# Kernel optimization log

Hardware: AMD Instinct MI355X
Metric: run time of the kernel (lower is better)

The kernel has to match this reference:

```python
import jax, jax.numpy as jnp
import numpy as np

T, B, IN, H, L = 128, 512, 512, 512, 2


def setup_inputs() -> dict:
    key = jax.random.key(0)
    ks = jax.random.split(key, 8)
    inp = {
        "latent": jax.random.normal(ks[0], (T, B, IN), jnp.float32),
        "h0": jax.random.normal(ks[1], (L, B, H), jnp.float32),
        "c0": jax.random.normal(ks[2], (L, B, H), jnp.float32),
        "reset_mask": jax.random.randint(ks[3], (T, B), 0, 2, jnp.int32),
    }
    # LSTM params, torch layout: W_ih (4H, in), W_hh (4H, H), biases (4H,) init to 1
    for l in range(L):
        in_l = IN if l == 0 else H
        k1, k2 = jax.random.split(jax.random.fold_in(key, 100 + l))
        inp[f"W_ih{l}"] = jax.random.normal(k1, (4 * H, in_l), jnp.float32) / np.float32(np.sqrt(in_l))
        inp[f"W_hh{l}"] = jax.random.normal(k2, (4 * H, H), jnp.float32) / np.float32(np.sqrt(H))
        inp[f"b_ih{l}"] = jnp.ones((4 * H,), jnp.float32)
        inp[f"b_hh{l}"] = jnp.ones((4 * H,), jnp.float32)
    return inp


def _cell(x, h, c, W_ih, W_hh, b_ih, b_hh):
    # torch gate order: input, forget, cell(g), output
    gates = x @ W_ih.T + b_ih + h @ W_hh.T + b_hh  # (B, 4H)
    i, f, g, o = jnp.split(gates, 4, axis=-1)
    i = jax.nn.sigmoid(i)
    f = jax.nn.sigmoid(f)
    g = jnp.tanh(g)
    o = jax.nn.sigmoid(o)
    c_new = f * c + i * g
    h_new = o * jnp.tanh(c_new)
    return h_new, c_new


def reference(latent, h0, c0, reset_mask,
              W_ih0, W_hh0, b_ih0, b_hh0,
              W_ih1, W_hh1, b_ih1, b_hh1):
    def step(carry, xs):
        h, c = carry  # (L, B, H) each
        x_t, m_t = xs
        m = (m_t != 0)[None, :, None]  # (1, B, 1), broadcast over layers and H
        h = jnp.where(m, 0.0, h)
        c = jnp.where(m, 0.0, c)
        h0n, c0n = _cell(x_t, h[0], c[0], W_ih0, W_hh0, b_ih0, b_hh0)
        h1n, c1n = _cell(h0n, h[1], c[1], W_ih1, W_hh1, b_ih1, b_hh1)
        return (jnp.stack([h0n, h1n]), jnp.stack([c0n, c1n])), h1n

    (h_n, c_n), hidden = jax.lax.scan(step, (h0, c0), (latent, reset_mask))
    return hidden, h_n, c_n  # hidden: (T, B, H)
```

## Files before the change

kernel.cpp:

```cpp
#include <hip/hip_runtime.h>
#include <hip/hip_bf16.h>

typedef __hip_bfloat16 bf16;
typedef unsigned short u16;
typedef unsigned long long u64;
using frag  = __attribute__((ext_vector_type(8))) short;
using f32x4 = __attribute__((ext_vector_type(4))) float;

static constexpr int T_  = 128;
static constexpr int B_  = 512;
static constexpr int H_  = 512;
static constexpr int K_  = 512;
static constexpr int G4_ = 2048;
static constexpr int NWG = 256;

static constexpr size_t W_BYTES = 131072;
static constexpr size_t SMEM_BYTES = W_BYTES;


__global__ void k_f32_to_bf16_v4(const float4* __restrict__ src,
                                 ushort4* __restrict__ dst, int n4) {
  int i = blockIdx.x * blockDim.x + threadIdx.x;
  int stride = gridDim.x * blockDim.x;
  for (; i < n4; i += stride) {
    float4 v = src[i];
    ushort4 o;
    bf16 t0 = __float2bfloat16(v.x); o.x = *reinterpret_cast<u16*>(&t0);
    bf16 t1 = __float2bfloat16(v.y); o.y = *reinterpret_cast<u16*>(&t1);
    bf16 t2 = __float2bfloat16(v.z); o.z = *reinterpret_cast<u16*>(&t2);
    bf16 t3 = __float2bfloat16(v.w); o.w = *reinterpret_cast<u16*>(&t3);
    dst[i] = o;
  }
}

__global__ void k_bias(const float* __restrict__ bih0, const float* __restrict__ bhh0,
                       const float* __restrict__ bih1, const float* __restrict__ bhh1,
                       float* __restrict__ bsum0, float* __restrict__ bsum1) {
  int i = blockIdx.x * blockDim.x + threadIdx.x;
  if (i < G4_) {
    bsum0[i] = bih0[i] + bhh0[i];
    bsum1[i] = bih1[i] + bhh1[i];
  }
}

__global__ void k_init2(const float* __restrict__ h0,
                        u16* __restrict__ bufA0, u16* __restrict__ bufA1) {
  int i = blockIdx.x * blockDim.x + threadIdx.x;
  int n = B_ * H_;
  if (i < n) {
    bf16 a = __float2bfloat16(h0[i]);
    bf16 b = __float2bfloat16(h0[n + i]);
    bufA0[i] = *reinterpret_cast<u16*>(&a);
    bufA1[n + i] = *reinterpret_cast<u16*>(&b);
  }
}

__global__ void k_zero(int* p) {
  int i = blockIdx.x * blockDim.x + threadIdx.x;
  if (i < 256) p[i] = 0;
}

__global__ __launch_bounds__(512, 2)
void k_main(const u16* __restrict__ latb,
            const u16* __restrict__ W0i, const u16* __restrict__ W0h,
            const u16* __restrict__ W1i, const u16* __restrict__ W1h,
            const float* __restrict__ bs0, const float* __restrict__ bs1,
            const int* __restrict__ reset,
            const float* __restrict__ c0,
            u16* __restrict__ h0seq,
            u16* __restrict__ bufA0,
            u16* __restrict__ bufA1,
            float* __restrict__ hidden,
            float* __restrict__ hn,
            float* __restrict__ cn,
            int* __restrict__ arr) {
  extern __shared__ char smem_raw[];
  u16* wlds = (u16*)smem_raw;
  __shared__ float hstage[8][16][20];

  const int tid   = threadIdx.x;
  const int wg    = blockIdx.x;
  const int lb    = wg & 7;
  const int layer = lb >> 2;
  const int bg    = lb & 3;
  const int cg    = wg >> 3;
  const int hbase = cg * 16;
  const int rowbase = bg * 128;
  const int wave  = tid >> 6;
  const int lane  = tid & 63;
  const int r16   = lane & 15;
  const int kq    = lane >> 4;
  const int wrow_local = wave * 16;
  const int wrow0 = rowbase + wrow_local;

  const u16* Wih = layer ? W1i : W0i;
  const u16* Whh = layer ? W1h : W0h;
  const float* bs = layer ? bs1 : bs0;
  u16* bufA_self = layer ? bufA1 : bufA0;

  for (int it = 0; it < 16; ++it) {
    int c = it * 512 + tid;
    int fb = c >> 6, l = c & 63;
    int ni = fb >> 5, kslot = fb & 31;
    int col = hbase + (l & 15);
    int klocal = (kslot & 15) * 32 + (l >> 4) * 8;
    const u16* M = (kslot < 16) ? Wih : Whh;
    const u16* src = M + (size_t)(ni * H_ + col) * K_ + klocal;
    *(float4*)(wlds + ((size_t)c) * 8) = *(const float4*)src;
  }

  float bias[4];
  #pragma unroll
  for (int g = 0; g < 4; ++g) bias[g] = bs[g * H_ + hbase + r16];

  float creg[4];
  #pragma unroll
  for (int j = 0; j < 4; ++j)
    creg[j] = c0[((size_t)layer * B_ + (wrow0 + kq * 4 + j)) * H_ + hbase + r16];

  __syncthreads();

  for (int p = 0; p <= T_; ++p) {
    if (p) { asm volatile("buffer_inv sc0" ::: "memory"); }

    const int t = layer ? (p - 1) : p;
    const bool active = (t >= 0 && t < T_);
    float hnew_r[4], cnew_r[4];

    if (active) {
      const u16* X  = layer ? (h0seq + (size_t)t * B_ * H_)
                            : (latb + (size_t)t * B_ * K_);
      const u16* Hp = bufA_self + (size_t)(p & 1) * B_ * H_;
      u16* HnA      = bufA_self + (size_t)((p + 1) & 1) * B_ * H_;

      const int* rst_t = reset + (size_t)t * B_;
      const int ra0 = rst_t[wrow0 + r16];
      const u16* x0  = X  + (size_t)(wrow0 + r16) * K_ + kq * 8;
      const u16* hp0 = Hp + (size_t)(wrow0 + r16) * H_ + kq * 8;

      f32x4 acc[4] = {};
      const frag zf = {};

      #pragma unroll
      for (int s = 0; s < 16; ++s) {
        frag a  = *reinterpret_cast<const frag*>(x0 + s * 32);
        frag ah = ra0 ? zf : *reinterpret_cast<const frag*>(hp0 + s * 32);
        #pragma unroll
        for (int ni = 0; ni < 4; ++ni) {
          frag bx = *reinterpret_cast<const frag*>(
              wlds + ((size_t)((ni * 32 + s) * 64 + lane)) * 8);
          frag bh = *reinterpret_cast<const frag*>(
              wlds + ((size_t)((ni * 32 + 16 + s) * 64 + lane)) * 8);
          acc[ni] = __builtin_amdgcn_mfma_f32_16x16x32_bf16(a,  bx, acc[ni], 0, 0, 0);
          acc[ni] = __builtin_amdgcn_mfma_f32_16x16x32_bf16(ah, bh, acc[ni], 0, 0, 0);
        }
      }

      #pragma unroll
      for (int j = 0; j < 4; ++j) {
        const int rstj = rst_t[wrow0 + kq * 4 + j];
        float gi = acc[0][j] + bias[0];
        float gf = acc[1][j] + bias[1];
        float gg = acc[2][j] + bias[2];
        float go = acc[3][j] + bias[3];
        float iv = 1.f / (1.f + __expf(-gi));
        float fv = 1.f / (1.f + __expf(-gf));
        float gv = 1.f - 2.f / (__expf(2.f * gg) + 1.f);
        float ov = 1.f / (1.f + __expf(-go));
        float ce = rstj ? 0.f : creg[j];
        float cnew = fv * ce + iv * gv;
        float hnew = ov * (1.f - 2.f / (__expf(2.f * cnew) + 1.f));
        creg[j] = cnew;
        cnew_r[j] = cnew;
        hnew_r[j] = hnew;
        hstage[wave][kq * 4 + j][r16] = hnew;
      }

      {
        const int prow = lane >> 2;
        const int pc4  = lane & 3;
        float4 v = *reinterpret_cast<const float4*>(&hstage[wave][prow][pc4 * 4]);
        bf16 b0 = __float2bfloat16(v.x), b1 = __float2bfloat16(v.y);
        bf16 b2 = __float2bfloat16(v.z), b3 = __float2bfloat16(v.w);
        u64 pk = (u64)*reinterpret_cast<u16*>(&b0)
               | ((u64)*reinterpret_cast<u16*>(&b1) << 16)
               | ((u64)*reinterpret_cast<u16*>(&b2) << 32)
               | ((u64)*reinterpret_cast<u16*>(&b3) << 48);
        const size_t hoff = (size_t)(wrow0 + prow) * H_ + hbase + pc4 * 4;
        *(u64*)(HnA + hoff) = pk;
        if (layer == 0) {
          __hip_atomic_store((u64*)(h0seq + (size_t)t * B_ * H_ + hoff), pk,
                             __ATOMIC_RELAXED, __HIP_MEMORY_SCOPE_AGENT);
        }
      }
    }

    if (p < T_) {
      asm volatile("s_waitcnt vmcnt(0)" ::: "memory");
      __syncthreads();
      if (tid == 0)
        __hip_atomic_store(arr + wg, p + 1, __ATOMIC_RELAXED, __HIP_MEMORY_SCOPE_AGENT);
    }

    if (active) {
      float* hidden_t = hidden + (size_t)t * B_ * H_;
      #pragma unroll
      for (int j = 0; j < 4; ++j) {
        const size_t off = (size_t)(wrow0 + kq * 4 + j) * H_ + hbase + r16;
        if (layer) hidden_t[off] = hnew_r[j];
        if (t == T_ - 1) {
          hn[(size_t)layer * B_ * H_ + off] = hnew_r[j];
          cn[(size_t)layer * B_ * H_ + off] = cnew_r[j];
        }
      }
    }

    if (p < T_) {
      if (wave == 0) {
        const int slot = (lane >> 1) * 8 + (lane & 1) * 4 + bg;
        while (__hip_atomic_load(arr + slot, __ATOMIC_RELAXED,
                                 __HIP_MEMORY_SCOPE_AGENT) < p + 1)
          __builtin_amdgcn_s_sleep(2);
      }
      __syncthreads();
    }
  }
}


extern "C" void kernel_launch(void* const* d_in, const int* in_sizes, int n_in,
                              void* d_out, int out_size, void* d_ws, size_t ws_size,
                              hipStream_t stream) {
  (void)in_sizes; (void)n_in; (void)out_size; (void)ws_size;

  const float* latent = (const float*)d_in[0];
  const float* h0in   = (const float*)d_in[1];
  const float* c0in   = (const float*)d_in[2];
  const int*   reset  = (const int*)d_in[3];
  const float* W_ih0  = (const float*)d_in[4];
  const float* W_hh0  = (const float*)d_in[5];
  const float* b_ih0  = (const float*)d_in[6];
  const float* b_hh0  = (const float*)d_in[7];
  const float* W_ih1  = (const float*)d_in[8];
  const float* W_hh1  = (const float*)d_in[9];
  const float* b_ih1  = (const float*)d_in[10];
  const float* b_hh1  = (const float*)d_in[11];

  float* out    = (float*)d_out;
  float* hidden = out;
  float* hn     = out + (size_t)T_ * B_ * H_;
  float* cn     = hn + (size_t)2 * B_ * H_;

  char* ws = (char*)d_ws;
  u16* latb  = (u16*)ws;
  u16* wih0b = latb + (size_t)T_ * B_ * K_;
  u16* whh0b = wih0b + (size_t)G4_ * K_;
  u16* wih1b = whh0b + (size_t)G4_ * K_;
  u16* whh1b = wih1b + (size_t)G4_ * K_;
  float* bsum0 = (float*)(whh1b + (size_t)G4_ * K_);
  float* bsum1 = bsum0 + G4_;
  u16* h0seq = (u16*)(bsum1 + G4_);
  u16* bufA0 = h0seq + (size_t)T_ * B_ * H_;
  u16* bufA1 = bufA0 + (size_t)2 * B_ * H_;
  int* arr   = (int*)(bufA1 + (size_t)2 * B_ * H_);

  int n_lat4 = T_ * B_ * K_ / 4;
  k_f32_to_bf16_v4<<<2048, 256, 0, stream>>>((const float4*)latent, (ushort4*)latb, n_lat4);
  int n_w4 = G4_ * K_ / 4;
  k_f32_to_bf16_v4<<<256, 256, 0, stream>>>((const float4*)W_ih0, (ushort4*)wih0b, n_w4);
  k_f32_to_bf16_v4<<<256, 256, 0, stream>>>((const float4*)W_hh0, (ushort4*)whh0b, n_w4);
  k_f32_to_bf16_v4<<<256, 256, 0, stream>>>((const float4*)W_ih1, (ushort4*)wih1b, n_w4);
  k_f32_to_bf16_v4<<<256, 256, 0, stream>>>((const float4*)W_hh1, (ushort4*)whh1b, n_w4);
  k_bias<<<(G4_ + 255) / 256, 256, 0, stream>>>(b_ih0, b_hh0, b_ih1, b_hh1, bsum0, bsum1);
  k_init2<<<(B_ * H_ + 255) / 256, 256, 0, stream>>>(h0in, bufA0, bufA1);
  k_zero<<<1, 256, 0, stream>>>(arr);

  hipFuncSetAttribute((const void*)k_main, hipFuncAttributeMaxDynamicSharedMemorySize,
                      (int)SMEM_BYTES);
  void* args[] = { (void*)&latb, (void*)&wih0b, (void*)&whh0b, (void*)&wih1b, (void*)&whh1b,
                   (void*)&bsum0, (void*)&bsum1, (void*)&reset, (void*)&c0in,
                   (void*)&h0seq, (void*)&bufA0, (void*)&bufA1,
                   (void*)&hidden, (void*)&hn, (void*)&cn, (void*)&arr };
  hipLaunchCooperativeKernel((void*)k_main, dim3(NWG), dim3(512), args,
                             (unsigned int)SMEM_BYTES, stream);
}
```

Before: 1.385 ms.

## Prefetch next-step input fragments into registers and narrow inter-layer barrier waits

```diff
diff --git a/kernel.cpp b/kernel.cpp
--- a/kernel.cpp
+++ b/kernel.cpp
@@ -98,6 +98,9 @@
   const float* bs = layer ? bs1 : bs0;
   u16* bufA_self = layer ? bufA1 : bufA0;
 
+  const int slotL0own = (lane & 31) * 8 + bg;
+  const int slotL1own = (lane & 31) * 8 + 4 + bg;
+
   for (int it = 0; it < 16; ++it) {
     int c = it * 512 + tid;
     int fb = c >> 6, l = c & 63;
@@ -118,6 +121,14 @@
   for (int j = 0; j < 4; ++j)
     creg[j] = c0[((size_t)layer * B_ + (wrow0 + kq * 4 + j)) * H_ + hbase + r16];
 
+  frag xfr[16];
+  if (layer == 0) {
+    const u16* x0 = latb + (size_t)(wrow0 + r16) * K_ + kq * 8;
+    #pragma unroll
+    for (int s = 0; s < 16; ++s)
+      xfr[s] = *reinterpret_cast<const frag*>(x0 + s * 32);
+  }
+
   __syncthreads();
 
   for (int p = 0; p <= T_; ++p) {
@@ -128,14 +139,11 @@
     float hnew_r[4], cnew_r[4];
 
     if (active) {
-      const u16* X  = layer ? (h0seq + (size_t)t * B_ * H_)
-                            : (latb + (size_t)t * B_ * K_);
       const u16* Hp = bufA_self + (size_t)(p & 1) * B_ * H_;
       u16* HnA      = bufA_self + (size_t)((p + 1) & 1) * B_ * H_;
 
       const int* rst_t = reset + (size_t)t * B_;
       const int ra0 = rst_t[wrow0 + r16];
-      const u16* x0  = X  + (size_t)(wrow0 + r16) * K_ + kq * 8;
       const u16* hp0 = Hp + (size_t)(wrow0 + r16) * H_ + kq * 8;
 
       f32x4 acc[4] = {};
@@ -143,7 +151,6 @@
 
       #pragma unroll
       for (int s = 0; s < 16; ++s) {
-        frag a  = *reinterpret_cast<const frag*>(x0 + s * 32);
         frag ah = ra0 ? zf : *reinterpret_cast<const frag*>(hp0 + s * 32);
         #pragma unroll
         for (int ni = 0; ni < 4; ++ni) {
@@ -151,8 +158,8 @@
               wlds + ((size_t)((ni * 32 + s) * 64 + lane)) * 8);
           frag bh = *reinterpret_cast<const frag*>(
               wlds + ((size_t)((ni * 32 + 16 + s) * 64 + lane)) * 8);
-          acc[ni] = __builtin_amdgcn_mfma_f32_16x16x32_bf16(a,  bx, acc[ni], 0, 0, 0);
-          acc[ni] = __builtin_amdgcn_mfma_f32_16x16x32_bf16(ah, bh, acc[ni], 0, 0, 0);
+          acc[ni] = __builtin_amdgcn_mfma_f32_16x16x32_bf16(xfr[s], bx, acc[ni], 0, 0, 0);
+          acc[ni] = __builtin_amdgcn_mfma_f32_16x16x32_bf16(ah,     bh, acc[ni], 0, 0, 0);
         }
       }
 
@@ -216,8 +223,28 @@
     }
 
     if (p < T_) {
+      const int tn = layer ? p : (p + 1);
+      const bool nact = (tn < T_);
+
+      if (layer == 1 && nact) {
+        if (wave == 0) {
+          while (__hip_atomic_load(arr + slotL0own, __ATOMIC_RELAXED,
+                                   __HIP_MEMORY_SCOPE_AGENT) < p + 1)
+            __builtin_amdgcn_s_sleep(2);
+        }
+        __syncthreads();
+      }
+      if (nact) {
+        const u16* X = layer ? (h0seq + (size_t)tn * B_ * H_)
+                             : (latb + (size_t)tn * B_ * K_);
+        const u16* x0 = X + (size_t)(wrow0 + r16) * K_ + kq * 8;
+        #pragma unroll
+        for (int s = 0; s < 16; ++s)
+          xfr[s] = *reinterpret_cast<const frag*>(x0 + s * 32);
+      }
+
       if (wave == 0) {
-        const int slot = (lane >> 1) * 8 + (lane & 1) * 4 + bg;
+        const int slot = layer ? slotL1own : slotL0own;
         while (__hip_atomic_load(arr + slot, __ATOMIC_RELAXED,
                                  __HIP_MEMORY_SCOPE_AGENT) < p + 1)
           __builtin_amdgcn_s_sleep(2);
```

After: 1.400 ms. Within noise of the previous version (+1.1%).
